# Optimization experiments

Hardware: AMD Instinct MI355X
Metric: run time of the kernel (lower is better)

Reference implementation:

```python
import jax, jax.numpy as jnp
import numpy as np

SEG = 2048      # segment_length
RATE = 4        # dilated_rate
DIM = 768
LN_EPS = 1e-5


def _sparsify(x):
    # b (l s) d -> b l s d, take every RATE-th within segment, flatten back
    b, L, d = x.shape
    x = x.reshape(b, L // SEG, SEG, d)[:, :, ::RATE]
    return x.reshape(b, -1, d)


def _layernorm(x, gamma, beta):
    mu = jnp.mean(x, axis=-1, keepdims=True)
    var = jnp.mean(jnp.square(x - mu), axis=-1, keepdims=True)
    return (x - mu) / jnp.sqrt(var + LN_EPS) * gamma + beta


def setup_inputs() -> dict:
    key = jax.random.key(0)
    ks = jax.random.split(key, 6)
    B, L, D = 4, 8192, DIM
    return {
        "Q": jax.random.normal(ks[0], (B, L, D), dtype=jnp.float32),
        "K": jax.random.normal(ks[1], (B, L, D), dtype=jnp.float32),
        "V": jax.random.normal(ks[2], (B, L, D), dtype=jnp.float32),
        "Wq": jax.random.normal(ks[3], (D, D), dtype=jnp.float32) * (1.0 / np.sqrt(D)),
        "Wk": jax.random.normal(ks[4], (D, D), dtype=jnp.float32) * (1.0 / np.sqrt(D)),
        "Wv": jax.random.normal(ks[5], (D, D), dtype=jnp.float32) * (1.0 / np.sqrt(D)),
        "ln_gamma": jnp.ones((D,), dtype=jnp.float32),
        "ln_beta": jnp.zeros((D,), dtype=jnp.float32),
    }


def reference(Q, K, V, Wq, Wk, Wv, ln_gamma, ln_beta):
    # strided segment dilation gather
    q = _sparsify(Q)  # [B, Ls, D], Ls = L/SEG * ceil(SEG/RATE)
    k = _sparsify(K)
    v = _sparsify(V)
    # linear projections (torch Linear: y = x @ W.T, no bias)
    q = q @ Wq.T
    k = k @ Wk.T
    v = v @ Wv.T
    # qk LayerNorm (shared norm module)
    q = _layernorm(q, ln_gamma, ln_beta)
    k = _layernorm(k, ln_gamma, ln_beta)
    # scaled dot product attention (non-causal, default scale 1/sqrt(D))
    scale = 1.0 / np.sqrt(q.shape[-1]).astype(np.float32)
    attn = jax.nn.softmax(jnp.einsum('bqd,bkd->bqk', q, k) * scale, axis=-1)
    out = jnp.einsum('bqk,bkd->bqd', attn, v)
    # dropout is identity in eval mode; final softmax over feature dim (as in source)
    return jax.nn.softmax(out, axis=-1)
```

## Files before the change

### kernel.cpp

```cpp
#include <hip/hip_runtime.h>
#include <math.h>

#define SEGLEN 2048
#define SRATE 4
#define DIM 768
#define BATCH 4
#define LFULL 8192
#define LSP 2048
#define NROWS (BATCH * LSP)
#define LN_EPS 1e-5f
#define ATT_SCALE 0.03608439182435161f

typedef __attribute__((ext_vector_type(8))) short s16x8;
typedef __attribute__((ext_vector_type(4))) float f32x4;

__device__ __forceinline__ ushort f2bf(float f) {
    unsigned u = __float_as_uint(f);
    u += 0x7fffu + ((u >> 16) & 1u);
    return (ushort)(u >> 16);
}
__device__ __forceinline__ float bf2f(ushort h) {
    return __uint_as_float(((unsigned)h) << 16);
}

__global__ void pack_gather(const float* __restrict__ src, ushort* __restrict__ dst) {
    int idx = blockIdx.x * 256 + threadIdx.x;
    int r  = idx / (DIM / 4);
    int dg = idx - r * (DIM / 4);
    int bb = r >> 11;
    int s  = r & 2047;
    int seg = s >> 9;
    int j   = s & 511;
    long srow = (long)bb * LFULL + seg * SEGLEN + j * SRATE;
    float4 f = *(const float4*)(src + srow * DIM + dg * 4);
    ushort4 o;
    o.x = f2bf(f.x); o.y = f2bf(f.y); o.z = f2bf(f.z); o.w = f2bf(f.w);
    *(ushort4*)(dst + (long)r * DIM + dg * 4) = o;
}

__global__ void convert_bf(const float* __restrict__ src, ushort* __restrict__ dst) {
    int idx = blockIdx.x * 256 + threadIdx.x;
    float4 f = *(const float4*)(src + (long)idx * 4);
    ushort4 o;
    o.x = f2bf(f.x); o.y = f2bf(f.y); o.z = f2bf(f.z); o.w = f2bf(f.w);
    *(ushort4*)(dst + (long)idx * 4) = o;
}

#define GTILE 128
#define GBK 32
#define LDSP 40

template<int MODE>
__global__ __launch_bounds__(256) void gemm_bt(
    const ushort* __restrict__ Ag, const ushort* __restrict__ Bg,
    ushort* __restrict__ Cb, float* __restrict__ Cf, float* __restrict__ lsum,
    int M, int N, int K, long sA, long sB, long sC, int ldc, float scale)
{
    __shared__ ushort As[GTILE * LDSP];
    __shared__ ushort Bs[GTILE * LDSP];

    const int z = blockIdx.z;
    const ushort* A = Ag + (long)z * sA;
    const ushort* B = Bg + (long)z * sB;

    const int tid = threadIdx.x;
    const int rowBase = blockIdx.y * GTILE;
    const int colBase = blockIdx.x * GTILE;
    const int wid = tid >> 6, lane = tid & 63;
    const int wm = wid >> 1, wn = wid & 1;
    const int quad = lane >> 4, lr = lane & 15;

    f32x4 acc[4][4] = {};

    const int idx0 = tid;
    const int idx1 = tid + 256;

    for (int k0 = 0; k0 < K; k0 += GBK) {
        uint4 a0 = *(const uint4*)(A + (long)(rowBase + (idx0 >> 2)) * K + k0 + (idx0 & 3) * 8);
        uint4 a1 = *(const uint4*)(A + (long)(rowBase + (idx1 >> 2)) * K + k0 + (idx1 & 3) * 8);
        uint4 b0 = *(const uint4*)(B + (long)(colBase + (idx0 >> 2)) * K + k0 + (idx0 & 3) * 8);
        uint4 b1 = *(const uint4*)(B + (long)(colBase + (idx1 >> 2)) * K + k0 + (idx1 & 3) * 8);
        __syncthreads();
        *(uint4*)&As[(idx0 >> 2) * LDSP + (idx0 & 3) * 8] = a0;
        *(uint4*)&As[(idx1 >> 2) * LDSP + (idx1 & 3) * 8] = a1;
        *(uint4*)&Bs[(idx0 >> 2) * LDSP + (idx0 & 3) * 8] = b0;
        *(uint4*)&Bs[(idx1 >> 2) * LDSP + (idx1 & 3) * 8] = b1;
        __syncthreads();

        s16x8 af[4], bfm[4];
#pragma unroll
        for (int t = 0; t < 4; t++)
            af[t] = *(const s16x8*)&As[(wm * 64 + t * 16 + lr) * LDSP + quad * 8];
#pragma unroll
        for (int t = 0; t < 4; t++)
            bfm[t] = *(const s16x8*)&Bs[(wn * 64 + t * 16 + lr) * LDSP + quad * 8];
#pragma unroll
        for (int i = 0; i < 4; i++)
#pragma unroll
            for (int j = 0; j < 4; j++)
                acc[i][j] = __builtin_amdgcn_mfma_f32_16x16x32_bf16(af[i], bfm[j], acc[i][j], 0, 0, 0);
    }

    if (MODE == 0) {
        ushort* Cz = Cb + (long)z * sC;
#pragma unroll
        for (int i = 0; i < 4; i++) {
            int r0 = rowBase + wm * 64 + i * 16 + quad * 4;
#pragma unroll
            for (int j = 0; j < 4; j++) {
                int c = colBase + wn * 64 + j * 16 + lr;
#pragma unroll
                for (int reg = 0; reg < 4; reg++)
                    Cz[(long)(r0 + reg) * ldc + c] = f2bf(acc[i][j][reg]);
            }
        }
    } else if (MODE == 1) {
#pragma unroll
        for (int i = 0; i < 4; i++) {
            int r0 = rowBase + wm * 64 + i * 16 + quad * 4;
            int bidx = r0 >> 11;
            int jj = r0 & 2047;
            ushort* Cz = Cb + (long)bidx * DIM * LSP;
#pragma unroll
            for (int j = 0; j < 4; j++) {
                int c = colBase + wn * 64 + j * 16 + lr;
                ushort4 o;
                o.x = f2bf(acc[i][j][0]); o.y = f2bf(acc[i][j][1]);
                o.z = f2bf(acc[i][j][2]); o.w = f2bf(acc[i][j][3]);
                *(ushort4*)(Cz + (long)c * LSP + jj) = o;
            }
        }
    } else if (MODE == 2) {
        ushort* Cz = Cb + (long)z * sC;
        float* lz = lsum + (long)z * M;
#pragma unroll
        for (int i = 0; i < 4; i++) {
            int r0 = rowBase + wm * 64 + i * 16 + quad * 4;
#pragma unroll
            for (int reg = 0; reg < 4; reg++) {
                float s = 0.f;
#pragma unroll
                for (int j = 0; j < 4; j++) {
                    int c = colBase + wn * 64 + j * 16 + lr;
                    float e = expf(acc[i][j][reg] * scale);
                    s += e;
                    Cz[(long)(r0 + reg) * ldc + c] = f2bf(e);
                }
                for (int m = 1; m < 16; m <<= 1) s += __shfl_xor(s, m, 64);
                if (lr == 0) atomicAdd(&lz[r0 + reg], s);
            }
        }
    } else {
        float* Cz = Cf + (long)z * sC;
#pragma unroll
        for (int i = 0; i < 4; i++) {
            int r0 = rowBase + wm * 64 + i * 16 + quad * 4;
#pragma unroll
            for (int j = 0; j < 4; j++) {
                int c = colBase + wn * 64 + j * 16 + lr;
#pragma unroll
                for (int reg = 0; reg < 4; reg++)
                    Cz[(long)(r0 + reg) * ldc + c] = acc[i][j][reg];
            }
        }
    }
}

__global__ __launch_bounds__(256) void ln_inplace(
    ushort* __restrict__ X, const float* __restrict__ gamma,
    const float* __restrict__ beta)
{
    int wid = threadIdx.x >> 6, lane = threadIdx.x & 63;
    int row = blockIdx.x * 4 + wid;
    ushort* xp = X + (long)row * DIM;
    float v[12];
    float s = 0.f;
#pragma unroll
    for (int c = 0; c < 12; c++) { v[c] = bf2f(xp[c * 64 + lane]); s += v[c]; }
    for (int m = 1; m < 64; m <<= 1) s += __shfl_xor(s, m, 64);
    float mean = s * (1.0f / 768.0f);
    float q = 0.f;
#pragma unroll
    for (int c = 0; c < 12; c++) { float d = v[c] - mean; q += d * d; }
    for (int m = 1; m < 64; m <<= 1) q += __shfl_xor(q, m, 64);
    float rstd = rsqrtf(q * (1.0f / 768.0f) + LN_EPS);
#pragma unroll
    for (int c = 0; c < 12; c++) {
        int idx = c * 64 + lane;
        float y = (v[c] - mean) * rstd * gamma[idx] + beta[idx];
        xp[idx] = f2bf(y);
    }
}

__global__ __launch_bounds__(256) void final_softmax(
    const float* __restrict__ O, const float* __restrict__ l, float* __restrict__ out)
{
    int wid = threadIdx.x >> 6, lane = threadIdx.x & 63;
    int row = blockIdx.x * 4 + wid;
    const float* op = O + (long)row * DIM;
    float inv = 1.0f / l[row];
    float v[12]; float mx = -1e30f;
#pragma unroll
    for (int c = 0; c < 12; c++) { v[c] = op[c * 64 + lane] * inv; mx = fmaxf(mx, v[c]); }
    for (int m = 1; m < 64; m <<= 1) mx = fmaxf(mx, __shfl_xor(mx, m, 64));
    float s = 0.f;
#pragma unroll
    for (int c = 0; c < 12; c++) { v[c] = expf(v[c] - mx); s += v[c]; }
    for (int m = 1; m < 64; m <<= 1) s += __shfl_xor(s, m, 64);
    float invs = 1.0f / s;
#pragma unroll
    for (int c = 0; c < 12; c++) out[(long)row * DIM + c * 64 + lane] = v[c] * invs;
}

extern "C" void kernel_launch(void* const* d_in, const int* in_sizes, int n_in,
                              void* d_out, int out_size, void* d_ws, size_t ws_size,
                              hipStream_t stream)
{
    const float* Q  = (const float*)d_in[0];
    const float* K_ = (const float*)d_in[1];
    const float* V  = (const float*)d_in[2];
    const float* Wq = (const float*)d_in[3];
    const float* Wk = (const float*)d_in[4];
    const float* Wv = (const float*)d_in[5];
    const float* g  = (const float*)d_in[6];
    const float* b  = (const float*)d_in[7];
    float* out = (float*)d_out;

    char* ws = (char*)d_ws;
    ushort* Xq  = (ushort*)(ws + 0);
    ushort* Xk  = (ushort*)(ws + 12582912);
    ushort* Xv  = (ushort*)(ws + 25165824);
    ushort* Wqb = (ushort*)(ws + 37748736);
    ushort* Wkb = (ushort*)(ws + 38928384);
    ushort* Wvb = (ushort*)(ws + 40108032);
    ushort* qb  = (ushort*)(ws + 41287680);
    ushort* kb  = (ushort*)(ws + 53870592);
    ushort* vT  = (ushort*)(ws + 66453504);
    float*  O   = (float*)(ws + 79036416);
    float*  l   = (float*)(ws + 104202240);
    ushort* P   = (ushort*)(ws + 0);

    (void)in_sizes; (void)n_in; (void)out_size; (void)ws_size;

    hipMemsetAsync(l, 0, NROWS * sizeof(float), stream);

    pack_gather<<<6144, 256, 0, stream>>>(Q,  Xq);
    pack_gather<<<6144, 256, 0, stream>>>(K_, Xk);
    pack_gather<<<6144, 256, 0, stream>>>(V,  Xv);
    convert_bf<<<576, 256, 0, stream>>>(Wq, Wqb);
    convert_bf<<<576, 256, 0, stream>>>(Wk, Wkb);
    convert_bf<<<576, 256, 0, stream>>>(Wv, Wvb);

    {
        dim3 grid(DIM / GTILE, NROWS / GTILE, 2);
        gemm_bt<0><<<grid, 256, 0, stream>>>(Xq, Wqb, qb, nullptr, nullptr,
            NROWS, DIM, DIM, (long)NROWS * DIM, (long)DIM * DIM, (long)NROWS * DIM, DIM, 0.f);
    }
    {
        dim3 grid(DIM / GTILE, NROWS / GTILE, 1);
        gemm_bt<1><<<grid, 256, 0, stream>>>(Xv, Wvb, vT, nullptr, nullptr,
            NROWS, DIM, DIM, 0, 0, 0, DIM, 0.f);
    }
    ln_inplace<<<4096, 256, 0, stream>>>(qb, g, b);

    {
        dim3 grid(LSP / GTILE, LSP / GTILE, BATCH);
        gemm_bt<2><<<grid, 256, 0, stream>>>(qb, kb, P, nullptr, l,
            LSP, LSP, DIM, (long)LSP * DIM, (long)LSP * DIM, (long)LSP * LSP, LSP, ATT_SCALE);
    }
    {
        dim3 grid(DIM / GTILE, LSP / GTILE, BATCH);
        gemm_bt<3><<<grid, 256, 0, stream>>>(P, vT, nullptr, O, nullptr,
            LSP, DIM, LSP, (long)LSP * LSP, (long)DIM * LSP, (long)LSP * DIM, DIM, 0.f);
    }
    final_softmax<<<2048, 256, 0, stream>>>(O, l, out);
}
```

Baseline: 450.0 us.

## Use direct global-to-LDS loads, merge launches, and split-K the PV GEMM

GEMM tile loading now uses global_load_lds to copy 16-byte chunks straight into unpadded LDS, removing the register staging. The three gathers, the weight conversions and the Q/K/V projection GEMMs are each merged into single batched launches. The PV GEMM is split along K into two halves written to separate buffers, which final_softmax sums, doubling the grid for better occupancy. expf is swapped for __expf. Removing the LDS padding can introduce bank conflicts on fragment reads.

```diff
diff --git a/kernel.cpp b/kernel.cpp
--- a/kernel.cpp
+++ b/kernel.cpp
@@ -23,7 +23,16 @@
     return __uint_as_float(((unsigned)h) << 16);
 }
 
-__global__ void pack_gather(const float* __restrict__ src, ushort* __restrict__ dst) {
+__device__ __forceinline__ void ld_lds16(const ushort* g, ushort* l) {
+    __builtin_amdgcn_global_load_lds(
+        (const __attribute__((address_space(1))) void*)g,
+        (__attribute__((address_space(3))) void*)l, 16, 0, 0);
+}
+
+__global__ void pack3(const float* __restrict__ Q, const float* __restrict__ Ks,
+                      const float* __restrict__ V, ushort* __restrict__ X) {
+    const float* src = blockIdx.z == 0 ? Q : blockIdx.z == 1 ? Ks : V;
+    ushort* dst = X + (long)blockIdx.z * (NROWS * DIM);
     int idx = blockIdx.x * 256 + threadIdx.x;
     int r  = idx / (DIM / 4);
     int dg = idx - r * (DIM / 4);
@@ -38,7 +47,10 @@
     *(ushort4*)(dst + (long)r * DIM + dg * 4) = o;
 }
 
-__global__ void convert_bf(const float* __restrict__ src, ushort* __restrict__ dst) {
+__global__ void conv3(const float* __restrict__ Wq, const float* __restrict__ Wk,
+                      const float* __restrict__ Wv, ushort* __restrict__ W) {
+    const float* src = blockIdx.z == 0 ? Wq : blockIdx.z == 1 ? Wk : Wv;
+    ushort* dst = W + (long)blockIdx.z * (DIM * DIM);
     int idx = blockIdx.x * 256 + threadIdx.x;
     float4 f = *(const float4*)(src + (long)idx * 4);
     ushort4 o;
@@ -48,20 +60,23 @@
 
 #define GTILE 128
 #define GBK 32
-#define LDSP 40
 
 template<int MODE>
 __global__ __launch_bounds__(256) void gemm_bt(
     const ushort* __restrict__ Ag, const ushort* __restrict__ Bg,
-    ushort* __restrict__ Cb, float* __restrict__ Cf, float* __restrict__ lsum,
-    int M, int N, int K, long sA, long sB, long sC, int ldc, float scale)
-{
-    __shared__ ushort As[GTILE * LDSP];
-    __shared__ ushort Bs[GTILE * LDSP];
+    ushort* __restrict__ Cb, ushort* __restrict__ Cb2,
+    float* __restrict__ Cf, float* __restrict__ Cf2, float* __restrict__ lsum,
+    int M, int N, int K, int lda, int ldb, long sA, long sB, long sC,
+    int ldc, float scale)
+{
+    __shared__ ushort As[GTILE * GBK];
+    __shared__ ushort Bs[GTILE * GBK];
 
     const int z = blockIdx.z;
-    const ushort* A = Ag + (long)z * sA;
-    const ushort* B = Bg + (long)z * sB;
+    const int bz = (MODE == 3) ? (z >> 1) : z;
+    const int hz = (MODE == 3) ? (z & 1) : 0;
+    const ushort* A = Ag + (long)bz * sA + (long)hz * K;
+    const ushort* B = Bg + (long)bz * sB + (long)hz * K;
 
     const int tid = threadIdx.x;
     const int rowBase = blockIdx.y * GTILE;
@@ -72,28 +87,26 @@
 
     f32x4 acc[4][4] = {};
 
-    const int idx0 = tid;
-    const int idx1 = tid + 256;
+    const ushort* gA = A + (long)(rowBase + wid * 32 + (lane >> 2)) * lda + (lane & 3) * 8;
+    const ushort* gB = B + (long)(colBase + wid * 32 + (lane >> 2)) * ldb + (lane & 3) * 8;
+    ushort* lA = As + wid * 1024;
+    ushort* lB = Bs + wid * 1024;
 
     for (int k0 = 0; k0 < K; k0 += GBK) {
-        uint4 a0 = *(const uint4*)(A + (long)(rowBase + (idx0 >> 2)) * K + k0 + (idx0 & 3) * 8);
-        uint4 a1 = *(const uint4*)(A + (long)(rowBase + (idx1 >> 2)) * K + k0 + (idx1 & 3) * 8);
-        uint4 b0 = *(const uint4*)(B + (long)(colBase + (idx0 >> 2)) * K + k0 + (idx0 & 3) * 8);
-        uint4 b1 = *(const uint4*)(B + (long)(colBase + (idx1 >> 2)) * K + k0 + (idx1 & 3) * 8);
         __syncthreads();
-        *(uint4*)&As[(idx0 >> 2) * LDSP + (idx0 & 3) * 8] = a0;
-        *(uint4*)&As[(idx1 >> 2) * LDSP + (idx1 & 3) * 8] = a1;
-        *(uint4*)&Bs[(idx0 >> 2) * LDSP + (idx0 & 3) * 8] = b0;
-        *(uint4*)&Bs[(idx1 >> 2) * LDSP + (idx1 & 3) * 8] = b1;
+        ld_lds16(gA + k0, lA);
+        ld_lds16(gA + 16 * lda + k0, lA + 512);
+        ld_lds16(gB + k0, lB);
+        ld_lds16(gB + 16 * ldb + k0, lB + 512);
         __syncthreads();
 
         s16x8 af[4], bfm[4];
 #pragma unroll
         for (int t = 0; t < 4; t++)
-            af[t] = *(const s16x8*)&As[(wm * 64 + t * 16 + lr) * LDSP + quad * 8];
+            af[t] = *(const s16x8*)&As[(wm * 64 + t * 16 + lr) * GBK + quad * 8];
 #pragma unroll
         for (int t = 0; t < 4; t++)
-            bfm[t] = *(const s16x8*)&Bs[(wn * 64 + t * 16 + lr) * LDSP + quad * 8];
+            bfm[t] = *(const s16x8*)&Bs[(wn * 64 + t * 16 + lr) * GBK + quad * 8];
 #pragma unroll
         for (int i = 0; i < 4; i++)
 #pragma unroll
@@ -102,32 +115,34 @@
     }
 
     if (MODE == 0) {
-        ushort* Cz = Cb + (long)z * sC;
-#pragma unroll
-        for (int i = 0; i < 4; i++) {
-            int r0 = rowBase + wm * 64 + i * 16 + quad * 4;
-#pragma unroll
-            for (int j = 0; j < 4; j++) {
-                int c = colBase + wn * 64 + j * 16 + lr;
-#pragma unroll
-                for (int reg = 0; reg < 4; reg++)
-                    Cz[(long)(r0 + reg) * ldc + c] = f2bf(acc[i][j][reg]);
-            }
-        }
-    } else if (MODE == 1) {
-#pragma unroll
-        for (int i = 0; i < 4; i++) {
-            int r0 = rowBase + wm * 64 + i * 16 + quad * 4;
-            int bidx = r0 >> 11;
-            int jj = r0 & 2047;
-            ushort* Cz = Cb + (long)bidx * DIM * LSP;
-#pragma unroll
-            for (int j = 0; j < 4; j++) {
-                int c = colBase + wn * 64 + j * 16 + lr;
-                ushort4 o;
-                o.x = f2bf(acc[i][j][0]); o.y = f2bf(acc[i][j][1]);
-                o.z = f2bf(acc[i][j][2]); o.w = f2bf(acc[i][j][3]);
-                *(ushort4*)(Cz + (long)c * LSP + jj) = o;
+        if (z < 2) {
+            ushort* Cz = Cb + (long)z * sC;
+#pragma unroll
+            for (int i = 0; i < 4; i++) {
+                int r0 = rowBase + wm * 64 + i * 16 + quad * 4;
+#pragma unroll
+                for (int j = 0; j < 4; j++) {
+                    int c = colBase + wn * 64 + j * 16 + lr;
+#pragma unroll
+                    for (int reg = 0; reg < 4; reg++)
+                        Cz[(long)(r0 + reg) * ldc + c] = f2bf(acc[i][j][reg]);
+                }
+            }
+        } else {
+#pragma unroll
+            for (int i = 0; i < 4; i++) {
+                int r0 = rowBase + wm * 64 + i * 16 + quad * 4;
+                int bidx = r0 >> 11;
+                int jj = r0 & 2047;
+                ushort* Cz = Cb2 + (long)bidx * DIM * LSP;
+#pragma unroll
+                for (int j = 0; j < 4; j++) {
+                    int c = colBase + wn * 64 + j * 16 + lr;
+                    ushort4 o;
+                    o.x = f2bf(acc[i][j][0]); o.y = f2bf(acc[i][j][1]);
+                    o.z = f2bf(acc[i][j][2]); o.w = f2bf(acc[i][j][3]);
+                    *(ushort4*)(Cz + (long)c * LSP + jj) = o;
+                }
             }
         }
     } else if (MODE == 2) {
@@ -142,7 +157,7 @@
 #pragma unroll
                 for (int j = 0; j < 4; j++) {
                     int c = colBase + wn * 64 + j * 16 + lr;
-                    float e = expf(acc[i][j][reg] * scale);
+                    float e = __expf(acc[i][j][reg] * scale);
                     s += e;
                     Cz[(long)(r0 + reg) * ldc + c] = f2bf(e);
                 }
@@ -151,7 +166,7 @@
             }
         }
     } else {
-        float* Cz = Cf + (long)z * sC;
+        float* Cz = (hz ? Cf2 : Cf) + (long)bz * sC;
 #pragma unroll
         for (int i = 0; i < 4; i++) {
             int r0 = rowBase + wm * 64 + i * 16 + quad * 4;
@@ -193,23 +208,27 @@
 }
 
 __global__ __launch_bounds__(256) void final_softmax(
-    const float* __restrict__ O, const float* __restrict__ l, float* __restrict__ out)
+    const float* __restrict__ O0, const float* __restrict__ O1,
+    const float* __restrict__ l, float* __restrict__ out)
 {
     int wid = threadIdx.x >> 6, lane = threadIdx.x & 63;
     int row = blockIdx.x * 4 + wid;
-    const float* op = O + (long)row * DIM;
+    long base = (long)row * DIM;
     float inv = 1.0f / l[row];
     float v[12]; float mx = -1e30f;
 #pragma unroll
-    for (int c = 0; c < 12; c++) { v[c] = op[c * 64 + lane] * inv; mx = fmaxf(mx, v[c]); }
+    for (int c = 0; c < 12; c++) {
+        v[c] = (O0[base + c * 64 + lane] + O1[base + c * 64 + lane]) * inv;
+        mx = fmaxf(mx, v[c]);
+    }
     for (int m = 1; m < 64; m <<= 1) mx = fmaxf(mx, __shfl_xor(mx, m, 64));
     float s = 0.f;
 #pragma unroll
-    for (int c = 0; c < 12; c++) { v[c] = expf(v[c] - mx); s += v[c]; }
+    for (int c = 0; c < 12; c++) { v[c] = __expf(v[c] - mx); s += v[c]; }
     for (int m = 1; m < 64; m <<= 1) s += __shfl_xor(s, m, 64);
     float invs = 1.0f / s;
 #pragma unroll
-    for (int c = 0; c < 12; c++) out[(long)row * DIM + c * 64 + lane] = v[c] * invs;
+    for (int c = 0; c < 12; c++) out[base + c * 64 + lane] = v[c] * invs;
 }
 
 extern "C" void kernel_launch(void* const* d_in, const int* in_sizes, int n_in,
@@ -228,50 +247,38 @@
 
     char* ws = (char*)d_ws;
     ushort* Xq  = (ushort*)(ws + 0);
-    ushort* Xk  = (ushort*)(ws + 12582912);
-    ushort* Xv  = (ushort*)(ws + 25165824);
     ushort* Wqb = (ushort*)(ws + 37748736);
-    ushort* Wkb = (ushort*)(ws + 38928384);
-    ushort* Wvb = (ushort*)(ws + 40108032);
     ushort* qb  = (ushort*)(ws + 41287680);
     ushort* kb  = (ushort*)(ws + 53870592);
     ushort* vT  = (ushort*)(ws + 66453504);
-    float*  O   = (float*)(ws + 79036416);
+    float*  O0  = (float*)(ws + 79036416);
     float*  l   = (float*)(ws + 104202240);
     ushort* P   = (ushort*)(ws + 0);
+    float*  O1  = (float*)(ws + 41287680);
 
     (void)in_sizes; (void)n_in; (void)out_size; (void)ws_size;
 
     hipMemsetAsync(l, 0, NROWS * sizeof(float), stream);
 
-    pack_gather<<<6144, 256, 0, stream>>>(Q,  Xq);
-    pack_gather<<<6144, 256, 0, stream>>>(K_, Xk);
-    pack_gather<<<6144, 256, 0, stream>>>(V,  Xv);
-    convert_bf<<<576, 256, 0, stream>>>(Wq, Wqb);
-    convert_bf<<<576, 256, 0, stream>>>(Wk, Wkb);
-    convert_bf<<<576, 256, 0, stream>>>(Wv, Wvb);
-
-    {
-        dim3 grid(DIM / GTILE, NROWS / GTILE, 2);
-        gemm_bt<0><<<grid, 256, 0, stream>>>(Xq, Wqb, qb, nullptr, nullptr,
-            NROWS, DIM, DIM, (long)NROWS * DIM, (long)DIM * DIM, (long)NROWS * DIM, DIM, 0.f);
-    }
-    {
-        dim3 grid(DIM / GTILE, NROWS / GTILE, 1);
-        gemm_bt<1><<<grid, 256, 0, stream>>>(Xv, Wvb, vT, nullptr, nullptr,
-            NROWS, DIM, DIM, 0, 0, 0, DIM, 0.f);
-    }
+    pack3<<<dim3(6144, 1, 3), 256, 0, stream>>>(Q, K_, V, Xq);
+    conv3<<<dim3(576, 1, 3), 256, 0, stream>>>(Wq, Wk, Wv, Wqb);
+
+    gemm_bt<0><<<dim3(DIM / GTILE, NROWS / GTILE, 3), 256, 0, stream>>>(
+        Xq, Wqb, qb, vT, nullptr, nullptr, nullptr,
+        NROWS, DIM, DIM, DIM, DIM,
+        (long)NROWS * DIM, (long)DIM * DIM, (long)NROWS * DIM, DIM, 0.f);
+
     ln_inplace<<<4096, 256, 0, stream>>>(qb, g, b);
 
-    {
-        dim3 grid(LSP / GTILE, LSP / GTILE, BATCH);
-        gemm_bt<2><<<grid, 256, 0, stream>>>(qb, kb, P, nullptr, l,
-            LSP, LSP, DIM, (long)LSP * DIM, (long)LSP * DIM, (long)LSP * LSP, LSP, ATT_SCALE);
-    }
-    {
-        dim3 grid(DIM / GTILE, LSP / GTILE, BATCH);
-        gemm_bt<3><<<grid, 256, 0, stream>>>(P, vT, nullptr, O, nullptr,
-            LSP, DIM, LSP, (long)LSP * LSP, (long)DIM * LSP, (long)LSP * DIM, DIM, 0.f);
-    }
-    final_softmax<<<2048, 256, 0, stream>>>(O, l, out);
-}
+    gemm_bt<2><<<dim3(LSP / GTILE, LSP / GTILE, BATCH), 256, 0, stream>>>(
+        qb, kb, P, nullptr, nullptr, nullptr, l,
+        LSP, LSP, DIM, DIM, DIM,
+        (long)LSP * DIM, (long)LSP * DIM, (long)LSP * LSP, LSP, ATT_SCALE);
+
+    gemm_bt<3><<<dim3(DIM / GTILE, LSP / GTILE, BATCH * 2), 256, 0, stream>>>(
+        P, vT, nullptr, nullptr, O0, O1, nullptr,
+        LSP, DIM, LSP / 2, LSP, LSP,
+        (long)LSP * LSP, (long)DIM * LSP, (long)LSP * DIM, DIM, 0.f);
+
+    final_softmax<<<2048, 256, 0, stream>>>(O0, O1, l, out);
+}
```

New measurement: 424.6 us. 5.6% less time.
